# Performance work log

Hardware: AMD Instinct MI355X
Metric: run time of the kernel (lower is better)

## Reference

```python
import jax, jax.numpy as jnp
import numpy as np

M, N, DIM, BATCH = 100, 100, 32, 128
GRID = M * N
ALPHA = 0.05
SIGMA = np.sqrt(GRID) / 2.0  # default sigma = sqrt(m*n)/2 = 50.0


def setup_inputs() -> dict:
    key = jax.random.key(0)
    k1, k2, k3 = jax.random.split(key, 3)
    x = jax.random.normal(k1, (BATCH, DIM), dtype=jnp.float32)
    centroids = jax.random.normal(k2, (GRID, DIM), dtype=jnp.float32)
    # grid locations [(i, j) for i in range(m) for j in range(n)]
    ii, jj = jnp.meshgrid(jnp.arange(M, dtype=jnp.int32), jnp.arange(N, dtype=jnp.int32), indexing='ij')
    locations = jnp.stack([ii.ravel(), jj.ravel()], axis=1)  # [GRID, 2]
    # precomputed non-periodic squared grid distances: [GRID, GRID]
    locf = locations.astype(jnp.float32)
    dr = locf[:, 0][:, None] - locf[:, 0][None, :]
    dc = locf[:, 1][:, None] - locf[:, 1][None, :]
    distance_mat = dr * dr + dc * dc
    learning_rate_op = jax.random.uniform(k3, (1,), dtype=jnp.float32) * 0.5 + 0.25
    return {"x": x, "centroids": centroids, "locations": locations,
            "distance_mat": distance_mat, "learning_rate_op": learning_rate_op}


def reference(x, centroids, locations, distance_mat, learning_rate_op):
    lr = learning_rate_op[0]
    # torch.cdist(x[:, None, :], centroids, p=2) -> [B, GRID]
    x2 = jnp.sum(x * x, axis=1, keepdims=True)            # [B, 1]
    c2 = jnp.sum(centroids * centroids, axis=1)           # [GRID]
    d2 = jnp.maximum(x2 + c2[None, :] - 2.0 * (x @ centroids.T), 0.0)
    dists = jnp.sqrt(d2)                                  # [B, GRID]
    mindist = jnp.min(dists, axis=-1)                     # [B]
    bmu_index = jnp.argmin(dists, axis=-1)                # [B]
    bmu_loc = locations[bmu_index]                        # [B, 2]
    alpha_op = ALPHA * lr
    sigma_op = SIGMA * lr
    # irregular gather of precomputed neighbourhood rows: [B, GRID]
    bmu_distance_squares = distance_mat[bmu_index]
    neighbourhood = jnp.exp(-bmu_distance_squares / (2.0 * sigma_op ** 2 + 1e-5))
    lrm = alpha_op * neighbourhood                        # [B, GRID]
    # delta = mean_b lrm[b,g] * (x[b,:] - centroids[g,:])  (no [B,GRID,DIM] temp)
    B = x.shape[0]
    delta = (jnp.einsum('bg,bd->gd', lrm, x) - jnp.sum(lrm, axis=0)[:, None] * centroids) / B
    new_weights = centroids + delta                       # [GRID, DIM]
    return bmu_loc, jnp.mean(mindist), new_weights
```

## Files before the change

### kernel.cpp

```cpp
#include <hip/hip_runtime.h>
#include <math.h>

#define BATCH 128
#define GRID_N 10000
#define DIM 32
#define MCOLS 100

__global__ __launch_bounds__(256) void k1_bmu(const float* __restrict__ x,
                                              const float* __restrict__ c,
                                              float* __restrict__ pmin,
                                              int* __restrict__ pidx) {
    const int blk   = blockIdx.x;
    const int bg    = blk >> 2;
    const int chunk = blk & 3;
    const int b0    = bg * 2;
    const int t     = threadIdx.x;

    float x0[DIM], x1[DIM];
#pragma unroll
    for (int d = 0; d < DIM; ++d) {
        x0[d] = x[b0 * DIM + d];
        x1[d] = x[(b0 + 1) * DIM + d];
    }

    const int gstart = chunk * 2500;
    const int gend   = gstart + 2500;

    float best0 = 3.4e38f, best1 = 3.4e38f;
    int   idx0 = 0, idx1 = 0;

    for (int g = gstart + t; g < gend; g += 256) {
        const float4* cr = (const float4*)(c + (size_t)g * DIM);
        float d0 = 0.f, d1 = 0.f;
#pragma unroll
        for (int k = 0; k < 8; ++k) {
            float4 cv = cr[k];
            float a;
            a = x0[4*k+0] - cv.x; d0 = fmaf(a, a, d0);
            a = x0[4*k+1] - cv.y; d0 = fmaf(a, a, d0);
            a = x0[4*k+2] - cv.z; d0 = fmaf(a, a, d0);
            a = x0[4*k+3] - cv.w; d0 = fmaf(a, a, d0);
            a = x1[4*k+0] - cv.x; d1 = fmaf(a, a, d1);
            a = x1[4*k+1] - cv.y; d1 = fmaf(a, a, d1);
            a = x1[4*k+2] - cv.z; d1 = fmaf(a, a, d1);
            a = x1[4*k+3] - cv.w; d1 = fmaf(a, a, d1);
        }
        if (d0 < best0) { best0 = d0; idx0 = g; }
        if (d1 < best1) { best1 = d1; idx1 = g; }
    }

#pragma unroll
    for (int m = 1; m < 64; m <<= 1) {
        float o0 = __shfl_xor(best0, m); int oi0 = __shfl_xor(idx0, m);
        if (o0 < best0 || (o0 == best0 && oi0 < idx0)) { best0 = o0; idx0 = oi0; }
        float o1 = __shfl_xor(best1, m); int oi1 = __shfl_xor(idx1, m);
        if (o1 < best1 || (o1 == best1 && oi1 < idx1)) { best1 = o1; idx1 = oi1; }
    }

    __shared__ float sm[2][4];
    __shared__ int   si[2][4];
    const int wave = t >> 6;
    const int lane = t & 63;
    if (lane == 0) {
        sm[0][wave] = best0; si[0][wave] = idx0;
        sm[1][wave] = best1; si[1][wave] = idx1;
    }
    __syncthreads();
    if (t == 0) {
        float bb = sm[0][0]; int bi = si[0][0];
        for (int w = 1; w < 4; ++w)
            if (sm[0][w] < bb || (sm[0][w] == bb && si[0][w] < bi)) { bb = sm[0][w]; bi = si[0][w]; }
        pmin[b0 * 4 + chunk] = bb;
        pidx[b0 * 4 + chunk] = bi;
        bb = sm[1][0]; bi = si[1][0];
        for (int w = 1; w < 4; ++w)
            if (sm[1][w] < bb || (sm[1][w] == bb && si[1][w] < bi)) { bb = sm[1][w]; bi = si[1][w]; }
        pmin[(b0 + 1) * 4 + chunk] = bb;
        pidx[(b0 + 1) * 4 + chunk] = bi;
    }
}

__global__ __launch_bounds__(128) void k2_final(const float* __restrict__ pmin,
                                                const int* __restrict__ pidx,
                                                const int* __restrict__ loc,
                                                float* __restrict__ out,
                                                int* __restrict__ bmuidx) {
    const int b = threadIdx.x;
    float best = pmin[b * 4];
    int   bi   = pidx[b * 4];
    for (int k = 1; k < 4; ++k) {
        float v = pmin[b * 4 + k];
        int   i = pidx[b * 4 + k];
        if (v < best || (v == best && i < bi)) { best = v; bi = i; }
    }
    out[2 * b]     = (float)loc[2 * bi];
    out[2 * b + 1] = (float)loc[2 * bi + 1];
    bmuidx[b] = bi;

    __shared__ float red[128];
    red[b] = sqrtf(fmaxf(best, 0.f));
    __syncthreads();
    for (int off = 64; off > 0; off >>= 1) {
        if (b < off) red[b] += red[b + off];
        __syncthreads();
    }
    if (b == 0) out[256] = red[0] * (1.0f / 128.0f);
}

__global__ __launch_bounds__(256) void k3_update(const float* __restrict__ x,
                                                 const float* __restrict__ c,
                                                 const int* __restrict__ loc,
                                                 const int* __restrict__ bmuidx,
                                                 const float* __restrict__ lrp,
                                                 float* __restrict__ out) {
    __shared__ float bi_s[BATCH], bj_s[BATCH];
    __shared__ float red[4][64][33];

    const int t = threadIdx.x;
    if (t < BATCH) {
        int idx = bmuidx[t];
        bi_s[t] = (float)loc[2 * idx];
        bj_s[t] = (float)loc[2 * idx + 1];
    }
    __syncthreads();

    const float lr    = lrp[0];
    const float alpha = 0.05f * lr;
    const float sig   = 50.0f * lr;
    const float inv   = 1.0f / (2.0f * sig * sig + 1e-5f);

    const int gl = t & 63;
    const int ch = t >> 6;
    const int g  = blockIdx.x * 64 + gl;
    const float gi = (float)(g / MCOLS);
    const float gj = (float)(g % MCOLS);

    float acc[DIM];
#pragma unroll
    for (int d = 0; d < DIM; ++d) acc[d] = 0.f;
    float s0 = 0.f;

    const int bbase = ch * 32;
    for (int i = 0; i < 32; ++i) {
        const int bu = __builtin_amdgcn_readfirstlane(bbase + i);
        const float dr = gi - bi_s[bu];
        const float dc = gj - bj_s[bu];
        const float w  = alpha * __expf(-fmaf(dr, dr, dc * dc) * inv);
        s0 += w;
        const float4* xr = (const float4*)(x + (size_t)bu * DIM);
#pragma unroll
        for (int k = 0; k < 8; ++k) {
            float4 xv = xr[k];
            acc[4*k+0] = fmaf(w, xv.x, acc[4*k+0]);
            acc[4*k+1] = fmaf(w, xv.y, acc[4*k+1]);
            acc[4*k+2] = fmaf(w, xv.z, acc[4*k+2]);
            acc[4*k+3] = fmaf(w, xv.w, acc[4*k+3]);
        }
    }

#pragma unroll
    for (int d = 0; d < DIM; ++d) red[ch][gl][d] = acc[d];
    red[ch][gl][32] = s0;
    __syncthreads();

    const int gl2  = t >> 2;
    const int part = t & 3;
    const int g2   = blockIdx.x * 64 + gl2;
    if (g2 < GRID_N) {
        const float ssum = red[0][gl2][32] + red[1][gl2][32] +
                           red[2][gl2][32] + red[3][gl2][32];
#pragma unroll
        for (int k = 0; k < 8; ++k) {
            const int d = part * 8 + k;
            const float a  = red[0][gl2][d] + red[1][gl2][d] +
                             red[2][gl2][d] + red[3][gl2][d];
            const float cg = c[(size_t)g2 * DIM + d];
            out[257 + (size_t)g2 * DIM + d] = cg + (a - ssum * cg) * (1.0f / 128.0f);
        }
    }
}

extern "C" void kernel_launch(void* const* d_in, const int* in_sizes, int n_in,
                              void* d_out, int out_size, void* d_ws, size_t ws_size,
                              hipStream_t stream) {
    const float* x   = (const float*)d_in[0];
    const float* c   = (const float*)d_in[1];
    const int*   loc = (const int*)d_in[2];
    const float* lrp = (const float*)d_in[4];
    float* out = (float*)d_out;

    float* pmin   = (float*)d_ws;
    int*   pidx   = (int*)((char*)d_ws + 512 * 4);
    int*   bmuidx = (int*)((char*)d_ws + 1024 * 4);

    hipLaunchKernelGGL(k1_bmu,   dim3(256), dim3(256), 0, stream, x, c, pmin, pidx);
    hipLaunchKernelGGL(k2_final, dim3(1),   dim3(128), 0, stream, pmin, pidx, loc, out, bmuidx);
    hipLaunchKernelGGL(k3_update, dim3(157), dim3(256), 0, stream, x, c, loc, bmuidx, lrp, out);
}
```

Measured before the change: 26.91 us.

## Fold BMU finalization into update kernel and retile BMU search

Removes the single-block finalize kernel: each update block now reduces the per-chunk partial minima itself to find BMU locations, and block 0 writes the locations and mean distance. The BMU search kernel now handles 4 batch rows per block over 8 grid chunks of 1250 instead of 2 rows over 4 chunks, reusing each centroid load across more rows. This cuts one kernel launch and its serialized dependency. In exchange, every update block redundantly does the small reduction, and the search kernel uses more registers.

```diff
diff --git a/kernel.cpp b/kernel.cpp
--- a/kernel.cpp
+++ b/kernel.cpp
@@ -5,124 +5,116 @@
 #define GRID_N 10000
 #define DIM 32
 #define MCOLS 100
+#define NCHUNK 8
+#define GCHUNK 1250
 
 __global__ __launch_bounds__(256) void k1_bmu(const float* __restrict__ x,
                                               const float* __restrict__ c,
                                               float* __restrict__ pmin,
                                               int* __restrict__ pidx) {
     const int blk   = blockIdx.x;
-    const int bg    = blk >> 2;
-    const int chunk = blk & 3;
-    const int b0    = bg * 2;
+    const int bg    = blk >> 3;
+    const int chunk = blk & 7;
+    const int b0    = bg * 4;
     const int t     = threadIdx.x;
 
-    float x0[DIM], x1[DIM];
+    float xr[4][DIM];
 #pragma unroll
-    for (int d = 0; d < DIM; ++d) {
-        x0[d] = x[b0 * DIM + d];
-        x1[d] = x[(b0 + 1) * DIM + d];
-    }
+    for (int i = 0; i < 4; ++i)
+#pragma unroll
+        for (int d = 0; d < DIM; ++d)
+            xr[i][d] = x[(b0 + i) * DIM + d];
 
-    const int gstart = chunk * 2500;
-    const int gend   = gstart + 2500;
+    const int gstart = chunk * GCHUNK;
+    const int gend   = gstart + GCHUNK;
 
-    float best0 = 3.4e38f, best1 = 3.4e38f;
-    int   idx0 = 0, idx1 = 0;
+    float best[4] = {3.4e38f, 3.4e38f, 3.4e38f, 3.4e38f};
+    int   idx[4]  = {0, 0, 0, 0};
 
     for (int g = gstart + t; g < gend; g += 256) {
         const float4* cr = (const float4*)(c + (size_t)g * DIM);
-        float d0 = 0.f, d1 = 0.f;
+        float d2[4] = {0.f, 0.f, 0.f, 0.f};
 #pragma unroll
         for (int k = 0; k < 8; ++k) {
             float4 cv = cr[k];
-            float a;
-            a = x0[4*k+0] - cv.x; d0 = fmaf(a, a, d0);
-            a = x0[4*k+1] - cv.y; d0 = fmaf(a, a, d0);
-            a = x0[4*k+2] - cv.z; d0 = fmaf(a, a, d0);
-            a = x0[4*k+3] - cv.w; d0 = fmaf(a, a, d0);
-            a = x1[4*k+0] - cv.x; d1 = fmaf(a, a, d1);
-            a = x1[4*k+1] - cv.y; d1 = fmaf(a, a, d1);
-            a = x1[4*k+2] - cv.z; d1 = fmaf(a, a, d1);
-            a = x1[4*k+3] - cv.w; d1 = fmaf(a, a, d1);
+#pragma unroll
+            for (int i = 0; i < 4; ++i) {
+                float a;
+                a = xr[i][4*k+0] - cv.x; d2[i] = fmaf(a, a, d2[i]);
+                a = xr[i][4*k+1] - cv.y; d2[i] = fmaf(a, a, d2[i]);
+                a = xr[i][4*k+2] - cv.z; d2[i] = fmaf(a, a, d2[i]);
+                a = xr[i][4*k+3] - cv.w; d2[i] = fmaf(a, a, d2[i]);
+            }
         }
-        if (d0 < best0) { best0 = d0; idx0 = g; }
-        if (d1 < best1) { best1 = d1; idx1 = g; }
+#pragma unroll
+        for (int i = 0; i < 4; ++i)
+            if (d2[i] < best[i]) { best[i] = d2[i]; idx[i] = g; }
     }
 
 #pragma unroll
     for (int m = 1; m < 64; m <<= 1) {
-        float o0 = __shfl_xor(best0, m); int oi0 = __shfl_xor(idx0, m);
-        if (o0 < best0 || (o0 == best0 && oi0 < idx0)) { best0 = o0; idx0 = oi0; }
-        float o1 = __shfl_xor(best1, m); int oi1 = __shfl_xor(idx1, m);
-        if (o1 < best1 || (o1 == best1 && oi1 < idx1)) { best1 = o1; idx1 = oi1; }
+#pragma unroll
+        for (int i = 0; i < 4; ++i) {
+            float o  = __shfl_xor(best[i], m);
+            int   oi = __shfl_xor(idx[i], m);
+            if (o < best[i] || (o == best[i] && oi < idx[i])) { best[i] = o; idx[i] = oi; }
+        }
     }
 
-    __shared__ float sm[2][4];
-    __shared__ int   si[2][4];
+    __shared__ float sm[4][4];
+    __shared__ int   si[4][4];
     const int wave = t >> 6;
     const int lane = t & 63;
     if (lane == 0) {
-        sm[0][wave] = best0; si[0][wave] = idx0;
-        sm[1][wave] = best1; si[1][wave] = idx1;
+#pragma unroll
+        for (int i = 0; i < 4; ++i) { sm[i][wave] = best[i]; si[i][wave] = idx[i]; }
     }
     __syncthreads();
-    if (t == 0) {
-        float bb = sm[0][0]; int bi = si[0][0];
+    if (t < 4) {
+        float bb = sm[t][0]; int bi = si[t][0];
+#pragma unroll
         for (int w = 1; w < 4; ++w)
-            if (sm[0][w] < bb || (sm[0][w] == bb && si[0][w] < bi)) { bb = sm[0][w]; bi = si[0][w]; }
-        pmin[b0 * 4 + chunk] = bb;
-        pidx[b0 * 4 + chunk] = bi;
-        bb = sm[1][0]; bi = si[1][0];
-        for (int w = 1; w < 4; ++w)
-            if (sm[1][w] < bb || (sm[1][w] == bb && si[1][w] < bi)) { bb = sm[1][w]; bi = si[1][w]; }
-        pmin[(b0 + 1) * 4 + chunk] = bb;
-        pidx[(b0 + 1) * 4 + chunk] = bi;
+            if (sm[t][w] < bb || (sm[t][w] == bb && si[t][w] < bi)) { bb = sm[t][w]; bi = si[t][w]; }
+        pmin[(b0 + t) * NCHUNK + chunk] = bb;
+        pidx[(b0 + t) * NCHUNK + chunk] = bi;
     }
-}
-
-__global__ __launch_bounds__(128) void k2_final(const float* __restrict__ pmin,
-                                                const int* __restrict__ pidx,
-                                                const int* __restrict__ loc,
-                                                float* __restrict__ out,
-                                                int* __restrict__ bmuidx) {
-    const int b = threadIdx.x;
-    float best = pmin[b * 4];
-    int   bi   = pidx[b * 4];
-    for (int k = 1; k < 4; ++k) {
-        float v = pmin[b * 4 + k];
-        int   i = pidx[b * 4 + k];
-        if (v < best || (v == best && i < bi)) { best = v; bi = i; }
-    }
-    out[2 * b]     = (float)loc[2 * bi];
-    out[2 * b + 1] = (float)loc[2 * bi + 1];
-    bmuidx[b] = bi;
-
-    __shared__ float red[128];
-    red[b] = sqrtf(fmaxf(best, 0.f));
-    __syncthreads();
-    for (int off = 64; off > 0; off >>= 1) {
-        if (b < off) red[b] += red[b + off];
-        __syncthreads();
-    }
-    if (b == 0) out[256] = red[0] * (1.0f / 128.0f);
 }
 
 __global__ __launch_bounds__(256) void k3_update(const float* __restrict__ x,
                                                  const float* __restrict__ c,
                                                  const int* __restrict__ loc,
-                                                 const int* __restrict__ bmuidx,
+                                                 const float* __restrict__ pmin,
+                                                 const int* __restrict__ pidx,
                                                  const float* __restrict__ lrp,
                                                  float* __restrict__ out) {
     __shared__ float bi_s[BATCH], bj_s[BATCH];
     __shared__ float red[4][64][33];
+    __shared__ float partial[2];
 
     const int t = threadIdx.x;
+
+    float msum = 0.f;
     if (t < BATCH) {
-        int idx = bmuidx[t];
-        bi_s[t] = (float)loc[2 * idx];
-        bj_s[t] = (float)loc[2 * idx + 1];
+        float best = pmin[t * NCHUNK];
+        int   bi   = pidx[t * NCHUNK];
+#pragma unroll
+        for (int k = 1; k < NCHUNK; ++k) {
+            float v = pmin[t * NCHUNK + k];
+            int   i = pidx[t * NCHUNK + k];
+            if (v < best || (v == best && i < bi)) { best = v; bi = i; }
+        }
+        const float li = (float)loc[2 * bi];
+        const float lj = (float)loc[2 * bi + 1];
+        bi_s[t] = li;
+        bj_s[t] = lj;
+        if (blockIdx.x == 0) { out[2 * t] = li; out[2 * t + 1] = lj; }
+        msum = sqrtf(fmaxf(best, 0.f));
     }
+#pragma unroll
+    for (int m = 1; m < 64; m <<= 1) msum += __shfl_xor(msum, m);
+    if (t < BATCH && (t & 63) == 0) partial[t >> 6] = msum;
     __syncthreads();
+    if (blockIdx.x == 0 && t == 0) out[256] = (partial[0] + partial[1]) * (1.0f / 128.0f);
 
     const float lr    = lrp[0];
     const float alpha = 0.05f * lr;
@@ -147,10 +139,10 @@
         const float dc = gj - bj_s[bu];
         const float w  = alpha * __expf(-fmaf(dr, dr, dc * dc) * inv);
         s0 += w;
-        const float4* xr = (const float4*)(x + (size_t)bu * DIM);
+        const float4* xrp = (const float4*)(x + (size_t)bu * DIM);
 #pragma unroll
         for (int k = 0; k < 8; ++k) {
-            float4 xv = xr[k];
+            float4 xv = xrp[k];
             acc[4*k+0] = fmaf(w, xv.x, acc[4*k+0]);
             acc[4*k+1] = fmaf(w, xv.y, acc[4*k+1]);
             acc[4*k+2] = fmaf(w, xv.z, acc[4*k+2]);
@@ -189,11 +181,9 @@
     const float* lrp = (const float*)d_in[4];
     float* out = (float*)d_out;
 
-    float* pmin   = (float*)d_ws;
-    int*   pidx   = (int*)((char*)d_ws + 512 * 4);
-    int*   bmuidx = (int*)((char*)d_ws + 1024 * 4);
+    float* pmin = (float*)d_ws;
+    int*   pidx = (int*)((char*)d_ws + 1024 * 4);
 
-    hipLaunchKernelGGL(k1_bmu,   dim3(256), dim3(256), 0, stream, x, c, pmin, pidx);
-    hipLaunchKernelGGL(k2_final, dim3(1),   dim3(128), 0, stream, pmin, pidx, loc, out, bmuidx);
-    hipLaunchKernelGGL(k3_update, dim3(157), dim3(256), 0, stream, x, c, loc, bmuidx, lrp, out);
+    hipLaunchKernelGGL(k1_bmu,    dim3(256), dim3(256), 0, stream, x, c, pmin, pidx);
+    hipLaunchKernelGGL(k3_update, dim3(157), dim3(256), 0, stream, x, c, loc, pmin, pidx, lrp, out);
 }
```

After: 23.12 us. 14.1% less time.
